# Kernel optimization log

Measured on AMD Instinct MI355X. Metric: run time of the kernel, lower is better.

## Reference

```python
import jax, jax.numpy as jnp
import numpy as np

# dims: N batch, C in-channels, T frames, V joints, H heads, HD per-head dim, O out-channels
N, C, T, V = 32, 64, 256, 25
H, HD, O = 8, 8, 64  # HD = max(C//8, 8)
SCALE = HD ** -0.5
EPS = 1e-5


def setup_inputs() -> dict:
    key = jax.random.key(0)
    ks = jax.random.split(key, 10)
    return {
        "x": jax.random.normal(ks[0], (N, C, T, V), jnp.float32),
        "ln_gamma": jnp.ones((C,), jnp.float32),
        "ln_beta": jnp.zeros((C,), jnp.float32),
        "w_qk": jax.random.normal(ks[1], (C, 2 * H * HD), jnp.float32),  # to_qk init N(0,1)
        "b_qk": jax.random.normal(ks[2], (2 * H * HD,), jnp.float32) * 0.02,
        "shared_topology": jax.random.uniform(ks[3], (H, V, V), jnp.float32),
        "conv_w": jax.random.normal(ks[4], (H, O, C), jnp.float32) * np.sqrt(2.0 / (O * H)),
        "conv_b": jnp.zeros((H, O), jnp.float32),
        "bn_gamma": jnp.full((O,), 1e-6, jnp.float32),
        "bn_beta": jnp.zeros((O,), jnp.float32),
        "bn_mean": jnp.zeros((O,), jnp.float32),
        "bn_var": jnp.ones((O,), jnp.float32),
    }


def reference(x, ln_gamma, ln_beta, w_qk, b_qk, shared_topology,
              conv_w, conv_b, bn_gamma, bn_beta, bn_mean, bn_var):
    # ---- SelfAttention over joints ----
    y = jnp.transpose(x, (0, 2, 3, 1))                 # [N,T,V,C]
    mu = jnp.mean(y, axis=-1, keepdims=True)
    var = jnp.var(y, axis=-1, keepdims=True)
    yn = (y - mu) * jax.lax.rsqrt(var + EPS) * ln_gamma + ln_beta
    qk = yn @ w_qk + b_qk                              # [N,T,V,2*H*HD]
    B = N * T
    q, k = jnp.split(qk.reshape(B, V, 2 * H * HD), 2, axis=-1)
    q = q.reshape(B, V, H, HD).transpose(0, 2, 1, 3)   # [B,H,V,HD]
    k = k.reshape(B, V, H, HD).transpose(0, 2, 1, 3)
    dots = jnp.einsum("bhid,bhjd->bhij", q, k) * SCALE
    attn = jax.nn.softmax(dots, axis=-1).astype(jnp.float32)  # [B,H,V,V]

    # ---- attention-gated graph conv ----
    A = attn * shared_topology[None]                   # [B,H,V,V]
    feat = jnp.transpose(x, (0, 2, 3, 1)).reshape(B, V, C)  # [B,V,C]
    z = jnp.einsum("bhuv,bvc->bhuc", A, feat)          # per-head aggregate [B,H,V,C]
    # fused per-head 1x1 convs + sum over heads
    out = jnp.einsum("bhuc,hoc->buo", z, conv_w) + conv_b.sum(0)  # [B,V,O]
    out = out.reshape(N, T, V, O).transpose(0, 3, 1, 2)           # [N,O,T,V]

    # ---- BatchNorm (inference-mode) + residual + ReLU ----
    g = (bn_gamma * jax.lax.rsqrt(bn_var + EPS))[None, :, None, None]
    b = (bn_beta - bn_mean * bn_gamma * jax.lax.rsqrt(bn_var + EPS))[None, :, None, None]
    out = out * g + b
    out = jax.nn.relu(out + x)  # down is identity (in_c == out_c)
    return out
```

## Files before the change

### kernel.cpp

```cpp
#include <hip/hip_runtime.h>
#include <math.h>

#define SCALE_L2E 0.51006972157f
#define EPSV 1e-5f

typedef __attribute__((ext_vector_type(8))) short bf16x8;
typedef __attribute__((ext_vector_type(4))) float f32x4;
typedef __attribute__((ext_vector_type(16))) float f32x16;
typedef __attribute__((ext_vector_type(4))) int i32x4;
typedef __attribute__((ext_vector_type(2))) int i32x2;

static __device__ __forceinline__ unsigned short bfh(float f) {
    return (unsigned short)(__builtin_bit_cast(unsigned int, f) >> 16);
}
static __device__ __forceinline__ float bf2f(unsigned short s) {
    return __builtin_bit_cast(float, (unsigned int)s << 16);
}
static __device__ __forceinline__ int pack2(float lo, float hi) {
    return __builtin_amdgcn_perm(__builtin_bit_cast(unsigned int, hi),
                                 __builtin_bit_cast(unsigned int, lo), 0x07060302u);
}
#define LGKM0() __asm__ __volatile__("s_waitcnt lgkmcnt(0)" ::: "memory")

__global__ void prep_kernel(const float* __restrict__ w_qk,
                            const float* __restrict__ conv_w,
                            const float* __restrict__ conv_b,
                            const float* __restrict__ bn_g, const float* __restrict__ bn_b,
                            const float* __restrict__ bn_m, const float* __restrict__ bn_v,
                            unsigned short* __restrict__ ws) {
    int i = blockIdx.x * 256 + threadIdx.x;
    if (i < 8192) {
        int f = i >> 9, rem = i & 511, l = rem >> 3, j = rem & 7;
        int nt = f >> 1, ks = f & 1;
        int k = ks * 32 + (l >> 4) * 8 + j;
        int nn = nt * 16 + (l & 15);
        ws[i] = bfh(w_qk[k * 128 + nn]);
    } else if (i < 40960) {
        int i2 = i - 8192;
        int g = i2 >> 9, rem = i2 & 511, l = rem >> 3, j = rem & 7;
        int h = g >> 3, nt = (g >> 1) & 3, ks = g & 1;
        int c = ks * 32 + (l >> 4) * 8 + j;
        int o = nt * 16 + (l & 15);
        ws[i] = bfh(conv_w[h * 4096 + o * 64 + c]);
    } else if (i < 41024) {
        int o = i - 40960;
        float gv = bn_g[o] * rsqrtf(bn_v[o] + EPSV);
        float bb = bn_b[o] - bn_m[o] * gv;
        float cb = 0.f;
        for (int h = 0; h < 8; h++) cb += conv_b[h * 64 + o];
        float* wsf = (float*)(ws + 40960);
        wsf[o] = gv;
        wsf[64 + o] = bb + cb * gv;
    }
}

__global__ __launch_bounds__(256, 3)
void sagc_kernel(const float* __restrict__ x,
                 const float* __restrict__ ln_g, const float* __restrict__ ln_b,
                 const float* __restrict__ b_qk,
                 const float* __restrict__ topo,
                 const unsigned short* __restrict__ ws,
                 float* __restrict__ out)
{
    __shared__ __align__(16) unsigned char smem[32768];
    const int tid = threadIdx.x;
    const int lane = tid & 63, wv = tid >> 6;
    const int l15 = lane & 15, quad = lane >> 4;
    const int r32 = lane & 31, hi = lane >> 5;

    unsigned char* my = smem + wv * 8192;
    unsigned short* qbuf = (unsigned short*)my;
    unsigned short* kbuf = (unsigned short*)(my + 1536);
    unsigned char*  fwb  = my;
    unsigned char*  ghb  = my + 4096;
    float*          mus  = (float*)(my + 4096);
    float*          rss  = mus + 32;

    const unsigned short* wqk = ws;
    const unsigned short* w2f = ws + 8192;
    const float* bnA = (const float*)(ws + 40960);
    const float* bnB = bnA + 64;

    const int tile = blockIdx.x * 4 + wv;
    const int n = tile >> 8, t = tile & 255;
    const float* xg = x + (size_t)n * 409600 + (size_t)t * 25;
    float* og = out + (size_t)n * 409600 + (size_t)t * 25;

    float xf[2][2][8];
    #pragma unroll
    for (int mt = 0; mt < 2; mt++) {
        const int v = mt * 16 + l15;
        const bool ok = (v < 25);
        const float* xc = xg + v;
        #pragma unroll
        for (int ks = 0; ks < 2; ks++)
            #pragma unroll
            for (int j = 0; j < 8; j++) {
                int c = ks * 32 + quad * 8 + j;
                xf[mt][ks][j] = ok ? xc[c * 6400] : 0.f;
            }
    }

    bf16x8 xa[2][2], sqf[2][2];
    #pragma unroll
    for (int mt = 0; mt < 2; mt++)
        #pragma unroll
        for (int ks = 0; ks < 2; ks++) {
            i32x4 pa, ps;
            #pragma unroll
            for (int q = 0; q < 4; q++) {
                float a = xf[mt][ks][2 * q], b = xf[mt][ks][2 * q + 1];
                pa[q] = pack2(a, b);
                ps[q] = pack2(a * a, b * b);
            }
            xa[mt][ks]  = __builtin_bit_cast(bf16x8, pa);
            sqf[mt][ks] = __builtin_bit_cast(bf16x8, ps);
        }

    {
        i32x4 ones_i = {0x3C803C80, 0x3C803C80, 0x3C803C80, 0x3C803C80};
        bf16x8 onesf = __builtin_bit_cast(bf16x8, ones_i);
        f32x4 z4 = {0.f, 0.f, 0.f, 0.f};
        f32x4 dmu[2], ds2[2];
        #pragma unroll
        for (int mt = 0; mt < 2; mt++) {
            dmu[mt] = __builtin_amdgcn_mfma_f32_16x16x32_bf16(xa[mt][0], onesf, z4, 0, 0, 0);
            dmu[mt] = __builtin_amdgcn_mfma_f32_16x16x32_bf16(xa[mt][1], onesf, dmu[mt], 0, 0, 0);
            ds2[mt] = __builtin_amdgcn_mfma_f32_16x16x32_bf16(sqf[mt][0], onesf, z4, 0, 0, 0);
            ds2[mt] = __builtin_amdgcn_mfma_f32_16x16x32_bf16(sqf[mt][1], onesf, ds2[mt], 0, 0, 0);
        }
        if (l15 == 0) {
            #pragma unroll
            for (int mt = 0; mt < 2; mt++)
                #pragma unroll
                for (int r = 0; r < 4; r++) {
                    int v = mt * 16 + quad * 4 + r;
                    float mu = dmu[mt][r];
                    float var = ds2[mt][r] - mu * mu;
                    mus[v] = mu;
                    rss[v] = rsqrtf(var + EPSV);
                }
        }
    }
    LGKM0();

    bf16x8 yna[2][2];
    {
        float muv[2] = {mus[l15], mus[16 + l15]};
        float rsv[2] = {rss[l15], rss[16 + l15]};
        #pragma unroll
        for (int ks = 0; ks < 2; ks++) {
            f32x4 ga = *(const f32x4*)&ln_g[ks * 32 + quad * 8];
            f32x4 gb = *(const f32x4*)&ln_g[ks * 32 + quad * 8 + 4];
            f32x4 ba = *(const f32x4*)&ln_b[ks * 32 + quad * 8];
            f32x4 bb = *(const f32x4*)&ln_b[ks * 32 + quad * 8 + 4];
            #pragma unroll
            for (int mt = 0; mt < 2; mt++) {
                float yv[8];
                #pragma unroll
                for (int j = 0; j < 8; j++) {
                    float g = (j < 4) ? ga[j] : gb[j - 4];
                    float bt = (j < 4) ? ba[j] : bb[j - 4];
                    yv[j] = (xf[mt][ks][j] - muv[mt]) * rsv[mt] * g + bt;
                }
                i32x4 p;
                #pragma unroll
                for (int q = 0; q < 4; q++) p[q] = pack2(yv[2 * q], yv[2 * q + 1]);
                yna[mt][ks] = __builtin_bit_cast(bf16x8, p);
            }
        }
    }

    f32x4 acc[2][4];
    #pragma unroll
    for (int mt = 0; mt < 2; mt++)
        #pragma unroll
        for (int nt = 0; nt < 4; nt++)
            acc[mt][nt] = (f32x4){0.f, 0.f, 0.f, 0.f};

    const f32x4 z4 = {0.f, 0.f, 0.f, 0.f};
    const bf16x8 z8 = {0, 0, 0, 0, 0, 0, 0, 0};

    const int sw4 = (l15 >> 2) & 3;
    const int blkA = ((r32 >> 3) ^ hi) << 4;
    unsigned char* gwA = ghb + hi * 256 + (r32 & 7) * 2 + blkA;
    unsigned char* gwB = ghb + hi * 256 + (r32 & 7) * 2 + (blkA ^ 32);
    unsigned char* w0p = fwb + ((((quad >> 1) ^ sw4)) << 4) + (quad & 1) * 8;
    unsigned char* w1p = fwb + (((((quad >> 1) ^ sw4)) ^ 2) << 4) + (quad & 1) * 8;
    unsigned char* brp = fwb + l15 * 64 + ((quad ^ sw4) << 4);

    for (int hp = 0; hp < 4; hp++) {
        #pragma unroll
        for (int tsel = 0; tsel < 2; tsel++) {
            int nt = tsel ? (4 + hp) : hp;
            bf16x8 b0 = *(const bf16x8*)&wqk[(nt * 2 + 0) * 512 + lane * 8];
            bf16x8 b1 = *(const bf16x8*)&wqk[(nt * 2 + 1) * 512 + lane * 8];
            float bias = b_qk[(tsel ? 64 : 0) + hp * 16 + l15];
            unsigned short* buf = tsel ? kbuf : qbuf;
            #pragma unroll
            for (int mt = 0; mt < 2; mt++) {
                f32x4 d = __builtin_amdgcn_mfma_f32_16x16x32_bf16(yna[mt][0], b0, z4, 0, 0, 0);
                d = __builtin_amdgcn_mfma_f32_16x16x32_bf16(yna[mt][1], b1, d, 0, 0, 0);
                #pragma unroll
                for (int r = 0; r < 4; r++) {
                    int u = mt * 16 + quad * 4 + r;
                    if (u < 25) {
                        float val = d[r] + bias;
                        if (!tsel) val *= SCALE_L2E;
                        buf[u * 24 + l15] = bfh(val);
                    }
                }
            }
        }
        LGKM0();

        #pragma unroll
        for (int hh = 0; hh < 2; hh++) {
            bf16x8 aq = z8, bk = z8;
            if (hi == 0) {
                aq = *(const bf16x8*)&qbuf[r32 * 24 + hh * 8];
                bk = *(const bf16x8*)&kbuf[r32 * 24 + hh * 8];
            }
            f32x16 dd = {0.f,0.f,0.f,0.f,0.f,0.f,0.f,0.f,0.f,0.f,0.f,0.f,0.f,0.f,0.f,0.f};
            dd = __builtin_amdgcn_mfma_f32_32x32x16_bf16(aq, bk, dd, 0, 0, 0);
            #pragma unroll
            for (int r = 0; r < 16; r++) {
                int ub = (r & 3) + 8 * (r >> 2);
                if (ub + 4 * hi < 25) {
                    unsigned char* p = (((r >> 2) & 1) ? gwB : gwA) + hh * 2048 + ub * 64;
                    *(unsigned short*)p = bfh(dd[r]);
                }
            }
        }
        LGKM0();

        {
            int smh = lane >> 5, su = lane & 31;
            if (su < 25) {
                unsigned char* rowb = ghb + smh * 2048 + su * 64;
                int sz = ((su >> 2) & 3) << 4;
                i32x4 ra = *(const i32x4*)(rowb + (sz ^ 0));
                i32x4 rb = *(const i32x4*)(rowb + (sz ^ 16));
                i32x4 rc = *(const i32x4*)(rowb + (sz ^ 32));
                float f[25];
                #pragma unroll
                for (int w = 0; w < 4; w++) {
                    f[2 * w]      = __builtin_bit_cast(float, (unsigned)ra[w] << 16);
                    f[2 * w + 1]  = __builtin_bit_cast(float, (unsigned)ra[w] & 0xFFFF0000u);
                    f[8 + 2 * w]  = __builtin_bit_cast(float, (unsigned)rb[w] << 16);
                    f[9 + 2 * w]  = __builtin_bit_cast(float, (unsigned)rb[w] & 0xFFFF0000u);
                    f[16 + 2 * w] = __builtin_bit_cast(float, (unsigned)rc[w] << 16);
                    f[17 + 2 * w] = __builtin_bit_cast(float, (unsigned)rc[w] & 0xFFFF0000u);
                }
                f[24] = bf2f(*(const unsigned short*)(rowb + (sz ^ 48)));
                float g12[12];
                #pragma unroll
                for (int i2 = 0; i2 < 12; i2++) g12[i2] = fmaxf(f[i2], f[i2 + 12]);
                #pragma unroll
                for (int i2 = 0; i2 < 6; i2++) g12[i2] = fmaxf(g12[i2], g12[i2 + 6]);
                float m = fmaxf(fmaxf(fmaxf(g12[0], g12[1]), fmaxf(g12[2], g12[3])),
                                fmaxf(fmaxf(g12[4], g12[5]), f[24]));
                float s0 = 0.f, s1 = 0.f, s2 = 0.f, s3 = 0.f;
                #pragma unroll
                for (int v = 0; v < 24; v += 4) {
                    f[v]     = __builtin_amdgcn_exp2f(f[v] - m);     s0 += f[v];
                    f[v + 1] = __builtin_amdgcn_exp2f(f[v + 1] - m); s1 += f[v + 1];
                    f[v + 2] = __builtin_amdgcn_exp2f(f[v + 2] - m); s2 += f[v + 2];
                    f[v + 3] = __builtin_amdgcn_exp2f(f[v + 3] - m); s3 += f[v + 3];
                }
                f[24] = __builtin_amdgcn_exp2f(f[24] - m);
                float inv = __builtin_amdgcn_rcpf(((s0 + s1) + (s2 + s3)) + f[24]);
                const float* tp = topo + (hp * 2 + smh) * 625 + su * 25;
                #pragma unroll
                for (int v = 0; v < 25; v++) f[v] = f[v] * inv * tp[v];
                int d[12];
                #pragma unroll
                for (int p = 0; p < 12; p++) d[p] = pack2(f[2 * p], f[2 * p + 1]);
                *(i32x4*)(rowb + (sz ^ 0))  = (i32x4){d[0], d[1], d[2], d[3]};
                *(i32x4*)(rowb + (sz ^ 16)) = (i32x4){d[4], d[5], d[6], d[7]};
                *(i32x4*)(rowb + (sz ^ 32)) = (i32x4){d[8], d[9], d[10], d[11]};
                *(i32x4*)(rowb + (sz ^ 48)) = (i32x4){pack2(f[24], 0.f), 0, 0, 0};
            }
        }
        LGKM0();

        #pragma unroll
        for (int hh = 0; hh < 2; hh++) {
            int h = hp * 2 + hh;
            #pragma unroll
            for (int nt = 0; nt < 4; nt++) {
                bf16x8 w0 = *(const bf16x8*)&w2f[((h * 4 + nt) * 2 + 0) * 512 + lane * 8];
                bf16x8 w1 = *(const bf16x8*)&w2f[((h * 4 + nt) * 2 + 1) * 512 + lane * 8];
                f32x4 dw0 = __builtin_amdgcn_mfma_f32_16x16x32_bf16(xa[0][0], w0, z4, 0, 0, 0);
                dw0 = __builtin_amdgcn_mfma_f32_16x16x32_bf16(xa[0][1], w1, dw0, 0, 0, 0);
                f32x4 dw1 = __builtin_amdgcn_mfma_f32_16x16x32_bf16(xa[1][0], w0, z4, 0, 0, 0);
                dw1 = __builtin_amdgcn_mfma_f32_16x16x32_bf16(xa[1][1], w1, dw1, 0, 0, 0);
                i32x2 q0 = {pack2(dw0[0], dw0[1]), pack2(dw0[2], dw0[3])};
                i32x2 q1 = {pack2(dw1[0], dw1[1]), pack2(dw1[2], dw1[3])};
                *(i32x2*)(w0p + nt * 1024 + l15 * 64) = q0;
                *(i32x2*)(w1p + nt * 1024 + l15 * 64) = q1;
            }
            LGKM0();
            unsigned char* agp = ghb + hh * 2048 + l15 * 64 + ((quad ^ sw4) << 4);
            bf16x8 ag0 = *(const bf16x8*)agp;
            bf16x8 ag1 = *(const bf16x8*)(agp + 1024);
            #pragma unroll
            for (int nt = 0; nt < 4; nt++) {
                bf16x8 br = *(const bf16x8*)(brp + nt * 1024);
                acc[0][nt] = __builtin_amdgcn_mfma_f32_16x16x32_bf16(ag0, br, acc[0][nt], 0, 0, 0);
                acc[1][nt] = __builtin_amdgcn_mfma_f32_16x16x32_bf16(ag1, br, acc[1][nt], 0, 0, 0);
            }
        }
    }

    #pragma unroll
    for (int nt = 0; nt < 4; nt++) {
        int o = nt * 16 + l15;
        float gA = bnA[o], gB = bnB[o];
        #pragma unroll
        for (int mt = 0; mt < 2; mt++) {
            int ub = mt * 16 + quad * 4;
            #pragma unroll
            for (int r = 0; r < 4; r++) {
                int u = ub + r;
                if (u < 25) {
                    float val = acc[mt][nt][r] * gA + gB + xg[o * 6400 + u];
                    og[o * 6400 + u] = fmaxf(val, 0.f);
                }
            }
        }
    }
}

extern "C" void kernel_launch(void* const* d_in, const int* in_sizes, int n_in,
                              void* d_out, int out_size, void* d_ws, size_t ws_size,
                              hipStream_t stream) {
    const float* x      = (const float*)d_in[0];
    const float* ln_g   = (const float*)d_in[1];
    const float* ln_b   = (const float*)d_in[2];
    const float* w_qk   = (const float*)d_in[3];
    const float* b_qk   = (const float*)d_in[4];
    const float* topo   = (const float*)d_in[5];
    const float* conv_w = (const float*)d_in[6];
    const float* conv_b = (const float*)d_in[7];
    const float* bn_g   = (const float*)d_in[8];
    const float* bn_b   = (const float*)d_in[9];
    const float* bn_m   = (const float*)d_in[10];
    const float* bn_v   = (const float*)d_in[11];
    float* outp = (float*)d_out;
    unsigned short* wsp = (unsigned short*)d_ws;

    hipLaunchKernelGGL(prep_kernel, dim3(161), dim3(256), 0, stream,
                       w_qk, conv_w, conv_b, bn_g, bn_b, bn_m, bn_v, wsp);
    hipLaunchKernelGGL(sagc_kernel, dim3(2048), dim3(256), 0, stream,
                       x, ln_g, ln_b, b_qk, topo, (const unsigned short*)wsp, outp);
}
```

Baseline: 190.9 us.

## Compute LayerNorm stats via shuffles and prefetch topology and conv weights earlier

Replaces the MFMA-with-ones LayerNorm reduction and its LDS round trip with in-register sums plus cross-lane xor shuffles. Topology rows and per-head conv weights are loaded into registers before the LDS waits, and the hp loop is fully unrolled, so global load latency can overlap softmax and MFMA work. Launch bounds drop from 3 to 2 waves-per-SIMD minimum, allowing more registers per thread but possibly lowering occupancy. One redundant LDS wait per head pair is also removed.

```diff
diff --git a/kernel.cpp b/kernel.cpp
--- a/kernel.cpp
+++ b/kernel.cpp
@@ -54,7 +54,7 @@
     }
 }
 
-__global__ __launch_bounds__(256, 3)
+__global__ __launch_bounds__(256, 2)
 void sagc_kernel(const float* __restrict__ x,
                  const float* __restrict__ ln_g, const float* __restrict__ ln_b,
                  const float* __restrict__ b_qk,
@@ -73,8 +73,6 @@
     unsigned short* kbuf = (unsigned short*)(my + 1536);
     unsigned char*  fwb  = my;
     unsigned char*  ghb  = my + 4096;
-    float*          mus  = (float*)(my + 4096);
-    float*          rss  = mus + 32;
 
     const unsigned short* wqk = ws;
     const unsigned short* w2f = ws + 8192;
@@ -101,73 +99,56 @@
             }
     }
 
-    bf16x8 xa[2][2], sqf[2][2];
+    bf16x8 xa[2][2];
+    float sum_[2] = {0.f, 0.f}, ssq_[2] = {0.f, 0.f};
     #pragma unroll
     for (int mt = 0; mt < 2; mt++)
         #pragma unroll
         for (int ks = 0; ks < 2; ks++) {
-            i32x4 pa, ps;
-            #pragma unroll
-            for (int q = 0; q < 4; q++) {
-                float a = xf[mt][ks][2 * q], b = xf[mt][ks][2 * q + 1];
-                pa[q] = pack2(a, b);
-                ps[q] = pack2(a * a, b * b);
-            }
-            xa[mt][ks]  = __builtin_bit_cast(bf16x8, pa);
-            sqf[mt][ks] = __builtin_bit_cast(bf16x8, ps);
-        }
-
-    {
-        i32x4 ones_i = {0x3C803C80, 0x3C803C80, 0x3C803C80, 0x3C803C80};
-        bf16x8 onesf = __builtin_bit_cast(bf16x8, ones_i);
-        f32x4 z4 = {0.f, 0.f, 0.f, 0.f};
-        f32x4 dmu[2], ds2[2];
+            i32x4 pa;
+            #pragma unroll
+            for (int q = 0; q < 4; q++)
+                pa[q] = pack2(xf[mt][ks][2 * q], xf[mt][ks][2 * q + 1]);
+            xa[mt][ks] = __builtin_bit_cast(bf16x8, pa);
+            #pragma unroll
+            for (int j = 0; j < 8; j++) {
+                float a = xf[mt][ks][j];
+                sum_[mt] += a;
+                ssq_[mt] += a * a;
+            }
+        }
+
+    float muv[2], rsv[2];
+    #pragma unroll
+    for (int mt = 0; mt < 2; mt++) {
+        sum_[mt] += __shfl_xor(sum_[mt], 16);
+        sum_[mt] += __shfl_xor(sum_[mt], 32);
+        ssq_[mt] += __shfl_xor(ssq_[mt], 16);
+        ssq_[mt] += __shfl_xor(ssq_[mt], 32);
+        muv[mt] = sum_[mt] * 0.015625f;
+        rsv[mt] = rsqrtf(ssq_[mt] * 0.015625f - muv[mt] * muv[mt] + EPSV);
+    }
+
+    bf16x8 yna[2][2];
+    #pragma unroll
+    for (int ks = 0; ks < 2; ks++) {
+        f32x4 ga = *(const f32x4*)&ln_g[ks * 32 + quad * 8];
+        f32x4 gb = *(const f32x4*)&ln_g[ks * 32 + quad * 8 + 4];
+        f32x4 ba = *(const f32x4*)&ln_b[ks * 32 + quad * 8];
+        f32x4 bb = *(const f32x4*)&ln_b[ks * 32 + quad * 8 + 4];
         #pragma unroll
         for (int mt = 0; mt < 2; mt++) {
-            dmu[mt] = __builtin_amdgcn_mfma_f32_16x16x32_bf16(xa[mt][0], onesf, z4, 0, 0, 0);
-            dmu[mt] = __builtin_amdgcn_mfma_f32_16x16x32_bf16(xa[mt][1], onesf, dmu[mt], 0, 0, 0);
-            ds2[mt] = __builtin_amdgcn_mfma_f32_16x16x32_bf16(sqf[mt][0], onesf, z4, 0, 0, 0);
-            ds2[mt] = __builtin_amdgcn_mfma_f32_16x16x32_bf16(sqf[mt][1], onesf, ds2[mt], 0, 0, 0);
-        }
-        if (l15 == 0) {
-            #pragma unroll
-            for (int mt = 0; mt < 2; mt++)
-                #pragma unroll
-                for (int r = 0; r < 4; r++) {
-                    int v = mt * 16 + quad * 4 + r;
-                    float mu = dmu[mt][r];
-                    float var = ds2[mt][r] - mu * mu;
-                    mus[v] = mu;
-                    rss[v] = rsqrtf(var + EPSV);
-                }
-        }
-    }
-    LGKM0();
-
-    bf16x8 yna[2][2];
-    {
-        float muv[2] = {mus[l15], mus[16 + l15]};
-        float rsv[2] = {rss[l15], rss[16 + l15]};
-        #pragma unroll
-        for (int ks = 0; ks < 2; ks++) {
-            f32x4 ga = *(const f32x4*)&ln_g[ks * 32 + quad * 8];
-            f32x4 gb = *(const f32x4*)&ln_g[ks * 32 + quad * 8 + 4];
-            f32x4 ba = *(const f32x4*)&ln_b[ks * 32 + quad * 8];
-            f32x4 bb = *(const f32x4*)&ln_b[ks * 32 + quad * 8 + 4];
-            #pragma unroll
-            for (int mt = 0; mt < 2; mt++) {
-                float yv[8];
-                #pragma unroll
-                for (int j = 0; j < 8; j++) {
-                    float g = (j < 4) ? ga[j] : gb[j - 4];
-                    float bt = (j < 4) ? ba[j] : bb[j - 4];
-                    yv[j] = (xf[mt][ks][j] - muv[mt]) * rsv[mt] * g + bt;
-                }
-                i32x4 p;
-                #pragma unroll
-                for (int q = 0; q < 4; q++) p[q] = pack2(yv[2 * q], yv[2 * q + 1]);
-                yna[mt][ks] = __builtin_bit_cast(bf16x8, p);
-            }
+            float yv[8];
+            #pragma unroll
+            for (int j = 0; j < 8; j++) {
+                float g = (j < 4) ? ga[j] : gb[j - 4];
+                float bt = (j < 4) ? ba[j] : bb[j - 4];
+                yv[j] = (xf[mt][ks][j] - muv[mt]) * rsv[mt] * g + bt;
+            }
+            i32x4 p;
+            #pragma unroll
+            for (int q = 0; q < 4; q++) p[q] = pack2(yv[2 * q], yv[2 * q + 1]);
+            yna[mt][ks] = __builtin_bit_cast(bf16x8, p);
         }
     }
 
@@ -189,6 +170,7 @@
     unsigned char* w1p = fwb + (((((quad >> 1) ^ sw4)) ^ 2) << 4) + (quad & 1) * 8;
     unsigned char* brp = fwb + l15 * 64 + ((quad ^ sw4) << 4);
 
+    #pragma unroll
     for (int hp = 0; hp < 4; hp++) {
         #pragma unroll
         for (int tsel = 0; tsel < 2; tsel++) {
@@ -232,10 +214,17 @@
                 }
             }
         }
-        LGKM0();
-
+
+        float tpv[25];
         {
-            int smh = lane >> 5, su = lane & 31;
+            const float* tp = topo + (hp * 2 + hi) * 625 + (r32 < 25 ? r32 : 0) * 25;
+            #pragma unroll
+            for (int v = 0; v < 25; v++) tpv[v] = tp[v];
+        }
+        LGKM0();
+
+        {
+            int smh = hi, su = r32;
             if (su < 25) {
                 unsigned char* rowb = ghb + smh * 2048 + su * 64;
                 int sz = ((su >> 2) & 3) << 4;
@@ -270,9 +259,8 @@
                 }
                 f[24] = __builtin_amdgcn_exp2f(f[24] - m);
                 float inv = __builtin_amdgcn_rcpf(((s0 + s1) + (s2 + s3)) + f[24]);
-                const float* tp = topo + (hp * 2 + smh) * 625 + su * 25;
-                #pragma unroll
-                for (int v = 0; v < 25; v++) f[v] = f[v] * inv * tp[v];
+                #pragma unroll
+                for (int v = 0; v < 25; v++) f[v] = f[v] * inv * tpv[v];
                 int d[12];
                 #pragma unroll
                 for (int p = 0; p < 12; p++) d[p] = pack2(f[2 * p], f[2 * p + 1]);
@@ -282,26 +270,63 @@
                 *(i32x4*)(rowb + (sz ^ 48)) = (i32x4){pack2(f[24], 0.f), 0, 0, 0};
             }
         }
-        LGKM0();
-
-        #pragma unroll
-        for (int hh = 0; hh < 2; hh++) {
-            int h = hp * 2 + hh;
+
+        bf16x8 w2e[8];
+        #pragma unroll
+        for (int nt = 0; nt < 4; nt++) {
+            int h = hp * 2;
+            w2e[2 * nt]     = *(const bf16x8*)&w2f[((h * 4 + nt) * 2 + 0) * 512 + lane * 8];
+            w2e[2 * nt + 1] = *(const bf16x8*)&w2f[((h * 4 + nt) * 2 + 1) * 512 + lane * 8];
+        }
+        LGKM0();
+
+        #pragma unroll
+        for (int nt = 0; nt < 4; nt++) {
+            f32x4 dw0 = __builtin_amdgcn_mfma_f32_16x16x32_bf16(xa[0][0], w2e[2 * nt], z4, 0, 0, 0);
+            dw0 = __builtin_amdgcn_mfma_f32_16x16x32_bf16(xa[0][1], w2e[2 * nt + 1], dw0, 0, 0, 0);
+            f32x4 dw1 = __builtin_amdgcn_mfma_f32_16x16x32_bf16(xa[1][0], w2e[2 * nt], z4, 0, 0, 0);
+            dw1 = __builtin_amdgcn_mfma_f32_16x16x32_bf16(xa[1][1], w2e[2 * nt + 1], dw1, 0, 0, 0);
+            i32x2 q0 = {pack2(dw0[0], dw0[1]), pack2(dw0[2], dw0[3])};
+            i32x2 q1 = {pack2(dw1[0], dw1[1]), pack2(dw1[2], dw1[3])};
+            *(i32x2*)(w0p + nt * 1024 + l15 * 64) = q0;
+            *(i32x2*)(w1p + nt * 1024 + l15 * 64) = q1;
+        }
+        bf16x8 w2o[8];
+        #pragma unroll
+        for (int nt = 0; nt < 4; nt++) {
+            int h = hp * 2 + 1;
+            w2o[2 * nt]     = *(const bf16x8*)&w2f[((h * 4 + nt) * 2 + 0) * 512 + lane * 8];
+            w2o[2 * nt + 1] = *(const bf16x8*)&w2f[((h * 4 + nt) * 2 + 1) * 512 + lane * 8];
+        }
+        LGKM0();
+
+        {
+            unsigned char* agp = ghb + l15 * 64 + ((quad ^ sw4) << 4);
+            bf16x8 ag0 = *(const bf16x8*)agp;
+            bf16x8 ag1 = *(const bf16x8*)(agp + 1024);
             #pragma unroll
             for (int nt = 0; nt < 4; nt++) {
-                bf16x8 w0 = *(const bf16x8*)&w2f[((h * 4 + nt) * 2 + 0) * 512 + lane * 8];
-                bf16x8 w1 = *(const bf16x8*)&w2f[((h * 4 + nt) * 2 + 1) * 512 + lane * 8];
-                f32x4 dw0 = __builtin_amdgcn_mfma_f32_16x16x32_bf16(xa[0][0], w0, z4, 0, 0, 0);
-                dw0 = __builtin_amdgcn_mfma_f32_16x16x32_bf16(xa[0][1], w1, dw0, 0, 0, 0);
-                f32x4 dw1 = __builtin_amdgcn_mfma_f32_16x16x32_bf16(xa[1][0], w0, z4, 0, 0, 0);
-                dw1 = __builtin_amdgcn_mfma_f32_16x16x32_bf16(xa[1][1], w1, dw1, 0, 0, 0);
-                i32x2 q0 = {pack2(dw0[0], dw0[1]), pack2(dw0[2], dw0[3])};
-                i32x2 q1 = {pack2(dw1[0], dw1[1]), pack2(dw1[2], dw1[3])};
-                *(i32x2*)(w0p + nt * 1024 + l15 * 64) = q0;
-                *(i32x2*)(w1p + nt * 1024 + l15 * 64) = q1;
-            }
-            LGKM0();
-            unsigned char* agp = ghb + hh * 2048 + l15 * 64 + ((quad ^ sw4) << 4);
+                bf16x8 br = *(const bf16x8*)(brp + nt * 1024);
+                acc[0][nt] = __builtin_amdgcn_mfma_f32_16x16x32_bf16(ag0, br, acc[0][nt], 0, 0, 0);
+                acc[1][nt] = __builtin_amdgcn_mfma_f32_16x16x32_bf16(ag1, br, acc[1][nt], 0, 0, 0);
+            }
+        }
+
+        #pragma unroll
+        for (int nt = 0; nt < 4; nt++) {
+            f32x4 dw0 = __builtin_amdgcn_mfma_f32_16x16x32_bf16(xa[0][0], w2o[2 * nt], z4, 0, 0, 0);
+            dw0 = __builtin_amdgcn_mfma_f32_16x16x32_bf16(xa[0][1], w2o[2 * nt + 1], dw0, 0, 0, 0);
+            f32x4 dw1 = __builtin_amdgcn_mfma_f32_16x16x32_bf16(xa[1][0], w2o[2 * nt], z4, 0, 0, 0);
+            dw1 = __builtin_amdgcn_mfma_f32_16x16x32_bf16(xa[1][1], w2o[2 * nt + 1], dw1, 0, 0, 0);
+            i32x2 q0 = {pack2(dw0[0], dw0[1]), pack2(dw0[2], dw0[3])};
+            i32x2 q1 = {pack2(dw1[0], dw1[1]), pack2(dw1[2], dw1[3])};
+            *(i32x2*)(w0p + nt * 1024 + l15 * 64) = q0;
+            *(i32x2*)(w1p + nt * 1024 + l15 * 64) = q1;
+        }
+        LGKM0();
+
+        {
+            unsigned char* agp = ghb + 2048 + l15 * 64 + ((quad ^ sw4) << 4);
             bf16x8 ag0 = *(const bf16x8*)agp;
             bf16x8 ag1 = *(const bf16x8*)(agp + 1024);
             #pragma unroll
```

Result: faster. 185.9 us (-2.6%).
